# Optimization experiments

Hardware: AMD Instinct MI355X
Metric: run time of the kernel (lower is better)

The kernel has to match this reference:

```python
import jax, jax.numpy as jnp
import numpy as np

EMB = 384
GROUPS = 4
B, T = 32, 1024
MAX_DUR = 8
SILENCE_VAL = -11.5129251


def setup_inputs() -> dict:
    key = jax.random.key(0)
    k1, k2, k3, k4, k5 = jax.random.split(key, 5)
    phoneme = jax.random.normal(k1, (B, T, EMB), dtype=jnp.float32)
    durations = jax.random.randint(k2, (B, T + 1), 0, MAX_DUR, dtype=jnp.int32)
    t_out = int(np.asarray(jnp.sum(durations, axis=-1)).max())
    silence_token = jnp.full((EMB,), SILENCE_VAL, dtype=jnp.float32)
    # DurationPredictor params (grouped conv -> ReLU -> 1x1 conv to scalar)
    conv1_w = jax.random.normal(k3, (EMB, EMB // GROUPS, 3), dtype=jnp.float32) * 0.05
    conv1_b = jnp.zeros((EMB,), dtype=jnp.float32)
    conv2_w = jax.random.normal(k4, (1, EMB, 1), dtype=jnp.float32) * 0.05
    conv2_b = jnp.zeros((1,), dtype=jnp.float32)
    return {
        "phoneme": phoneme,
        "silence_token": silence_token,
        "conv1_w": conv1_w,
        "conv1_b": conv1_b,
        "conv2_w": conv2_w,
        "conv2_b": conv2_b,
        "durations": durations,
        "t_out": t_out,
    }


def _duration_predictor(x, conv1_w, conv1_b, conv2_w, conv2_b):
    # x: [B, Tp, E] -> durations_pred [B, Tp]
    xc = jnp.transpose(x, (0, 2, 1))  # [B, E, Tp]
    h = jax.lax.conv_general_dilated(
        xc, conv1_w, window_strides=(1,), padding=((1, 1),),
        dimension_numbers=("NCH", "OIH", "NCH"), feature_group_count=GROUPS)
    h = jax.nn.relu(h + conv1_b[None, :, None])
    d = jax.lax.conv_general_dilated(
        h, conv2_w, window_strides=(1,), padding=((0, 0),),
        dimension_numbers=("NCH", "OIH", "NCH"))
    return d[:, 0, :] + conv2_b[0]  # [B, Tp]


def _regulate(phoneme, durations, t_out):
    # Equivalent to the one-hot mask matmul: frame t gets token j where
    # cumsum[j-1] <= t < cumsum[j]; frames past total length are zero.
    cum = jnp.cumsum(durations, axis=-1)  # [B, Tp]
    pos = jnp.arange(t_out, dtype=cum.dtype)  # [t_out]
    idx = jax.vmap(lambda c: jnp.searchsorted(c, pos, side="right"))(cum)  # [B, t_out]
    valid = pos[None, :] < cum[:, -1:]
    idx = jnp.clip(idx, 0, phoneme.shape[1] - 1)
    gathered = jnp.take_along_axis(phoneme, idx[..., None], axis=1)  # [B, t_out, E]
    return jnp.where(valid[..., None], gathered, jnp.zeros((), phoneme.dtype))


def reference(phoneme, silence_token, conv1_w, conv1_b, conv2_w, conv2_b, durations, t_out):
    Bn = phoneme.shape[0]
    silence = jnp.broadcast_to(silence_token[None, None, :], (Bn, 1, phoneme.shape[2]))
    ph = jnp.concatenate((phoneme, silence), axis=1)  # [B, T+1, E]
    durations_pred = _duration_predictor(ph, conv1_w, conv1_b, conv2_w, conv2_b)
    expanded = _regulate(ph, durations, t_out)  # [B, t_out, E]
    return expanded, durations_pred
```

## Files before the change

kernel.cpp:

```cpp
#include <hip/hip_runtime.h>

#define BATCH 32
#define T_IN 1024
#define TP 1025
#define EMB 384
#define GROUPS 4
#define GC 96

typedef __attribute__((ext_vector_type(8))) short short8;
typedef __attribute__((ext_vector_type(4))) float f32x4;

#define N_WPACK (GROUPS * 9 * 6 * 64 * 8)
#define PREP_BLOCKS ((N_WPACK + 255) / 256)

__device__ __forceinline__ unsigned short f2bf(float f) {
    union { float f; unsigned u; } v; v.f = f;
    unsigned u = v.u + 0x7fffu + ((v.u >> 16) & 1u);
    return (unsigned short)(u >> 16);
}

__global__ __launch_bounds__(256) void prep_scan_kernel(const float* __restrict__ w1,
                                                        const int* __restrict__ dur,
                                                        unsigned short* __restrict__ wpack,
                                                        unsigned short* __restrict__ idx,
                                                        int t_out) {
    __shared__ int scum[TP];
    const int tid = threadIdx.x;

    if (blockIdx.x < PREP_BLOCKS) {
        int i = blockIdx.x * 256 + tid;
        if (i >= N_WPACK) return;
        int j = i & 7;
        int lane = (i >> 3) & 63;
        int rest = i >> 9;
        int nt = rest % 6; rest /= 6;
        int ks = rest % 9;
        int g = rest / 9;
        int oc = nt * 16 + (lane & 15);
        int kk = ks * 32 + (lane >> 4) * 8 + j;
        int k = kk / 96, ic = kk % 96;
        wpack[i] = f2bf(w1[((size_t)(g * GC + oc) * GC + ic) * 3 + k]);
        return;
    }

    const int b = blockIdx.x - PREP_BLOCKS;
    if (tid < 64) {
        const int* d = dur + b * TP;
        int offset = 0;
        for (int r = 0; r < 17; ++r) {
            int i2 = r * 64 + tid;
            int v = (i2 < TP) ? d[i2] : 0;
            int s = v;
#pragma unroll
            for (int off = 1; off < 64; off <<= 1) {
                int n = __shfl_up(s, off, 64);
                if (tid >= off) s += n;
            }
            if (i2 < TP) scum[i2] = s + offset;
            offset += __shfl(s, 63, 64);
        }
    }
    __syncthreads();

    unsigned short* ib = idx + (size_t)b * t_out;
    for (int j = tid; j < TP; j += 256) {
        int c = scum[j];
        int lo = j ? scum[j - 1] : 0;
        for (int f = lo; f < c; ++f) ib[f] = (unsigned short)j;
    }
    const int total = scum[TP - 1];
    for (int t = total + tid; t < t_out; t += 256) ib[t] = 0xFFFFu;
}

__global__ __launch_bounds__(256) void conv_mfma_kernel(const float* __restrict__ phoneme,
                                                        const float* __restrict__ silence,
                                                        const float* __restrict__ b1,
                                                        const float* __restrict__ w2,
                                                        const float* __restrict__ b2,
                                                        const unsigned short* __restrict__ wpack,
                                                        float* __restrict__ pred) {
    const int tile = blockIdx.x;
    const int b = blockIdx.y;
    const int t0 = tile * 64;

    __shared__ __align__(16) unsigned short xs[66][392];
    __shared__ float red[4][64];

    const int tid = threadIdx.x;

    for (int e = tid; e < 66 * 96; e += 256) {
        int row = e / 96;
        int v = e - row * 96;
        int r = t0 - 1 + row;
        float4 val;
        if (r < 0 || r > T_IN) {
            val = make_float4(0.f, 0.f, 0.f, 0.f);
        } else if (r == T_IN) {
            val = *(const float4*)(silence + v * 4);
        } else {
            val = *(const float4*)(phoneme + ((size_t)(b * T_IN + r)) * EMB + v * 4);
        }
        ushort4 pk;
        pk.x = f2bf(val.x); pk.y = f2bf(val.y); pk.z = f2bf(val.z); pk.w = f2bf(val.w);
        *(ushort4*)&xs[row][v * 4] = pk;
    }
    __syncthreads();

    const int g = tid >> 6;
    const int lane = tid & 63;
    const int quad = lane >> 4;
    const int lr = lane & 15;

    f32x4 acc[4][6];
#pragma unroll
    for (int mt = 0; mt < 4; ++mt)
#pragma unroll
        for (int nt = 0; nt < 6; ++nt) acc[mt][nt] = (f32x4){0.f, 0.f, 0.f, 0.f};

    const unsigned short* wg = wpack + (size_t)g * 9 * 6 * 512;

#pragma unroll
    for (int ks = 0; ks < 9; ++ks) {
        const int tap = ks / 3;
        const int col = g * GC + 32 * (ks % 3) + quad * 8;
        short8 a[4];
#pragma unroll
        for (int mt = 0; mt < 4; ++mt)
            a[mt] = *(const short8*)&xs[mt * 16 + lr + tap][col];
#pragma unroll
        for (int nt = 0; nt < 6; ++nt) {
            short8 bf = *(const short8*)(wg + ((size_t)(ks * 6 + nt) * 64 + lane) * 8);
#pragma unroll
            for (int mt = 0; mt < 4; ++mt)
                acc[mt][nt] = __builtin_amdgcn_mfma_f32_16x16x32_bf16(a[mt], bf, acc[mt][nt], 0, 0, 0);
        }
    }

    float s[4][4];
#pragma unroll
    for (int mt = 0; mt < 4; ++mt)
#pragma unroll
        for (int reg = 0; reg < 4; ++reg) s[mt][reg] = 0.f;
#pragma unroll
    for (int nt = 0; nt < 6; ++nt) {
        int oc = g * GC + nt * 16 + lr;
        float bias = b1[oc];
        float wc = w2[oc];
#pragma unroll
        for (int mt = 0; mt < 4; ++mt)
#pragma unroll
            for (int reg = 0; reg < 4; ++reg) {
                float h = acc[mt][nt][reg] + bias;
                h = h > 0.f ? h : 0.f;
                s[mt][reg] += wc * h;
            }
    }
#pragma unroll
    for (int off = 1; off < 16; off <<= 1)
#pragma unroll
        for (int mt = 0; mt < 4; ++mt)
#pragma unroll
            for (int reg = 0; reg < 4; ++reg)
                s[mt][reg] += __shfl_xor(s[mt][reg], off, 64);
#pragma unroll
    for (int mt = 0; mt < 4; ++mt)
#pragma unroll
        for (int reg = 0; reg < 4; ++reg)
            if (lr == mt * 4 + reg) red[g][mt * 16 + quad * 4 + reg] = s[mt][reg];
    __syncthreads();

    if (tid < 64) {
        int t = t0 + tid;
        if (t < TP)
            pred[b * TP + t] = red[0][tid] + red[1][tid] + red[2][tid] + red[3][tid] + b2[0];
    }
}

__global__ __launch_bounds__(256) void gather_kernel(const float* __restrict__ phoneme,
                                                     const float* __restrict__ silence,
                                                     const unsigned short* __restrict__ idx,
                                                     float* __restrict__ out,
                                                     int t_out) {
    const int b = blockIdx.y;
    const int nfe = t_out * 96;
    int e = (blockIdx.x * 256 + threadIdx.x) * 2;
    if (e >= nfe) return;
    int fl = e / 96;
    int v = e - fl * 96;
    unsigned short id = idx[(size_t)b * t_out + fl];
    f32x4 v0, v1;
    if (id == 0xFFFFu) {
        v0 = (f32x4){0.f, 0.f, 0.f, 0.f};
        v1 = v0;
    } else if (id == T_IN) {
        const f32x4* s4 = (const f32x4*)silence;
        v0 = s4[v]; v1 = s4[v + 1];
    } else {
        const f32x4* p = (const f32x4*)phoneme + ((size_t)b * T_IN + id) * 96 + v;
        v0 = p[0]; v1 = p[1];
    }
    f32x4* o = (f32x4*)out + (size_t)b * nfe + e;
    __builtin_nontemporal_store(v0, o);
    __builtin_nontemporal_store(v1, o + 1);
}

extern "C" void kernel_launch(void* const* d_in, const int* in_sizes, int n_in,
                              void* d_out, int out_size, void* d_ws, size_t ws_size,
                              hipStream_t stream) {
    const float* phoneme = (const float*)d_in[0];
    const float* silence = (const float*)d_in[1];
    const float* conv1_w = (const float*)d_in[2];
    const float* conv1_b = (const float*)d_in[3];
    const float* conv2_w = (const float*)d_in[4];
    const float* conv2_b = (const float*)d_in[5];
    const int* durations = (const int*)d_in[6];
    const int t_out = (out_size - BATCH * TP) / (BATCH * EMB);

    float* out_expanded = (float*)d_out;
    float* out_pred = (float*)d_out + (size_t)BATCH * t_out * EMB;

    unsigned short* idx = (unsigned short*)d_ws;
    size_t idx_bytes = ((size_t)BATCH * t_out * sizeof(unsigned short) + 255) & ~(size_t)255;
    unsigned short* wpack = (unsigned short*)((char*)d_ws + idx_bytes);

    prep_scan_kernel<<<PREP_BLOCKS + BATCH, 256, 0, stream>>>(
        conv1_w, durations, wpack, idx, t_out);
    conv_mfma_kernel<<<dim3(17, BATCH), 256, 0, stream>>>(
        phoneme, silence, conv1_b, conv2_w, conv2_b, wpack, out_pred);
    gather_kernel<<<dim3((t_out * 96 / 2 + 255) / 256, BATCH), 256, 0, stream>>>(
        phoneme, silence, idx, out_expanded, t_out);
}
```

Before: 295.6 us.

## Fuse conv and gather into one launch with grid-stride gather blocks

Merges the MFMA conv kernel and the gather kernel into a single launch, where the first 17 x-blocks per batch do the conv and the remaining blocks do the length-regulation gather. Each gather block now loops with a grid stride and handles about four times as many elements, which cuts the block count. This removes one kernel launch and lets the conv and gather work overlap on the GPU. In exchange, the gather stores are no longer nontemporal, which may pollute cache. The conv blocks also allocate large shared memory that the gather blocks do not need, which may limit occupancy for the gather part.

```diff
diff --git a/kernel.cpp b/kernel.cpp
--- a/kernel.cpp
+++ b/kernel.cpp
@@ -12,6 +12,7 @@
 
 #define N_WPACK (GROUPS * 9 * 6 * 64 * 8)
 #define PREP_BLOCKS ((N_WPACK + 255) / 256)
+#define CONV_TILES 17
 
 __device__ __forceinline__ unsigned short f2bf(float f) {
     union { float f; unsigned u; } v; v.f = f;
@@ -72,21 +73,50 @@
     for (int t = total + tid; t < t_out; t += 256) ib[t] = 0xFFFFu;
 }
 
-__global__ __launch_bounds__(256) void conv_mfma_kernel(const float* __restrict__ phoneme,
-                                                        const float* __restrict__ silence,
-                                                        const float* __restrict__ b1,
-                                                        const float* __restrict__ w2,
-                                                        const float* __restrict__ b2,
-                                                        const unsigned short* __restrict__ wpack,
-                                                        float* __restrict__ pred) {
-    const int tile = blockIdx.x;
-    const int b = blockIdx.y;
-    const int t0 = tile * 64;
-
+__global__ __launch_bounds__(256) void conv_gather_kernel(const float* __restrict__ phoneme,
+                                                          const float* __restrict__ silence,
+                                                          const float* __restrict__ b1,
+                                                          const float* __restrict__ w2,
+                                                          const float* __restrict__ b2,
+                                                          const unsigned short* __restrict__ wpack,
+                                                          const unsigned short* __restrict__ idx,
+                                                          float* __restrict__ pred,
+                                                          float* __restrict__ out,
+                                                          int t_out, int gx) {
     __shared__ __align__(16) unsigned short xs[66][392];
     __shared__ float red[4][64];
 
+    const int b = blockIdx.y;
     const int tid = threadIdx.x;
+
+    if (blockIdx.x >= CONV_TILES) {
+        const int bx = blockIdx.x - CONV_TILES;
+        const int P = t_out * 48;
+        const unsigned short* ib = idx + (size_t)b * t_out;
+        const f32x4* ph = (const f32x4*)phoneme + (size_t)b * T_IN * 96;
+        const f32x4* s4 = (const f32x4*)silence;
+        f32x4* ob = (f32x4*)out + (size_t)b * t_out * 96;
+        for (int p = bx * 256 + tid; p < P; p += gx * 256) {
+            int fl = p / 48;
+            int v = (p - fl * 48) * 2;
+            unsigned short id = ib[fl];
+            f32x4 v0, v1;
+            if (id == 0xFFFFu) {
+                v0 = (f32x4){0.f, 0.f, 0.f, 0.f};
+                v1 = v0;
+            } else if (id == T_IN) {
+                v0 = s4[v]; v1 = s4[v + 1];
+            } else {
+                const f32x4* pp = ph + (size_t)id * 96 + v;
+                v0 = pp[0]; v1 = pp[1];
+            }
+            f32x4* o = ob + (size_t)fl * 96 + v;
+            o[0] = v0; o[1] = v1;
+        }
+        return;
+    }
+
+    const int t0 = blockIdx.x * 64;
 
     for (int e = tid; e < 66 * 96; e += 256) {
         int row = e / 96;
@@ -176,34 +206,6 @@
     }
 }
 
-__global__ __launch_bounds__(256) void gather_kernel(const float* __restrict__ phoneme,
-                                                     const float* __restrict__ silence,
-                                                     const unsigned short* __restrict__ idx,
-                                                     float* __restrict__ out,
-                                                     int t_out) {
-    const int b = blockIdx.y;
-    const int nfe = t_out * 96;
-    int e = (blockIdx.x * 256 + threadIdx.x) * 2;
-    if (e >= nfe) return;
-    int fl = e / 96;
-    int v = e - fl * 96;
-    unsigned short id = idx[(size_t)b * t_out + fl];
-    f32x4 v0, v1;
-    if (id == 0xFFFFu) {
-        v0 = (f32x4){0.f, 0.f, 0.f, 0.f};
-        v1 = v0;
-    } else if (id == T_IN) {
-        const f32x4* s4 = (const f32x4*)silence;
-        v0 = s4[v]; v1 = s4[v + 1];
-    } else {
-        const f32x4* p = (const f32x4*)phoneme + ((size_t)b * T_IN + id) * 96 + v;
-        v0 = p[0]; v1 = p[1];
-    }
-    f32x4* o = (f32x4*)out + (size_t)b * nfe + e;
-    __builtin_nontemporal_store(v0, o);
-    __builtin_nontemporal_store(v1, o + 1);
-}
-
 extern "C" void kernel_launch(void* const* d_in, const int* in_sizes, int n_in,
                               void* d_out, int out_size, void* d_ws, size_t ws_size,
                               hipStream_t stream) {
@@ -223,10 +225,12 @@
     size_t idx_bytes = ((size_t)BATCH * t_out * sizeof(unsigned short) + 255) & ~(size_t)255;
     unsigned short* wpack = (unsigned short*)((char*)d_ws + idx_bytes);
 
+    const int P = t_out * 48;
+    const int gx = (P + 1023) / 1024;
+
     prep_scan_kernel<<<PREP_BLOCKS + BATCH, 256, 0, stream>>>(
         conv1_w, durations, wpack, idx, t_out);
-    conv_mfma_kernel<<<dim3(17, BATCH), 256, 0, stream>>>(
-        phoneme, silence, conv1_b, conv2_w, conv2_b, wpack, out_pred);
-    gather_kernel<<<dim3((t_out * 96 / 2 + 255) / 256, BATCH), 256, 0, stream>>>(
-        phoneme, silence, idx, out_expanded, t_out);
-}
+    conv_gather_kernel<<<dim3(CONV_TILES + gx, BATCH), 256, 0, stream>>>(
+        phoneme, silence, conv1_b, conv2_w, conv2_b, wpack, idx,
+        out_pred, out_expanded, t_out, gx);
+}
```

After: 301.5 us. 1.02x slower.
